# Kernel optimization log

Measured on AMD Instinct MI355X. Metric: run time of the kernel, lower is better.

Reference implementation:

```python
import jax, jax.numpy as jnp
import numpy as np

# ---- MPDM social-force hyperparameters (the `param` object in the torch code) ----
N = 4096            # number of agents (agent 0 = robot)
PED_SPEED = 1.5     # param.pedestrians_speed (max / desired speed, m/s)
ROBOT_SPEED = 1.5   # param.robot_speed
K = 2.0             # param.k   (goal-attraction relaxation gain)
ALPHA = 10.0        # param.alpha (repulsive force amplitude)
PED_RADIUS = 0.3    # param.ped_radius
PED_MASS = 60.0     # param.ped_mass
BETTA = 0.71        # param.betta (repulsive range)
DT = 0.4            # param.DT
A_COST = 4.0        # param.a (progress weight)
B_COST = 1.2        # param.b (blame range)
E_COST = 0.001      # param.e (numerical epsilon)
EPS = 1e-8


def setup_inputs() -> dict:
    key = jax.random.key(0)
    k1, k2, k3, k4 = jax.random.split(key, 4)
    pos = jax.random.normal(k1, (N, 2), dtype=jnp.float32) * 10.0   # spread agents over ~20x20 m
    vel = jax.random.normal(k2, (N, 2), dtype=jnp.float32) * 0.5
    state = jnp.concatenate([pos, vel], axis=1)                     # [N,4] = (x, y, vx, vy)
    goals = jax.random.normal(k3, (N, 2), dtype=jnp.float32) * 10.0
    cost = jnp.zeros((N, 1), dtype=jnp.float32)
    stacked = state                                                 # trajectory stack seed
    robot_init_pose = jax.random.normal(k4, (2,), dtype=jnp.float32) * 10.0
    return {"state": state, "cost": cost,
            "stacked_trajectories_for_visualizer": stacked,
            "goals": goals, "robot_init_pose": robot_init_pose}


def calc_forces(state, goals):
    pos = state[:, 0:2]
    vel = state[:, 2:4]
    # --- attractive force: relax toward desired velocity pointing at goal ---
    to_goal = goals - pos                                   # [N,2]
    dist_goal = jnp.linalg.norm(to_goal, axis=1, keepdims=True)
    e_goal = to_goal / (dist_goal + EPS)
    desired_speed = jnp.full((N, 1), PED_SPEED, dtype=state.dtype).at[0, 0].set(ROBOT_SPEED)
    attr_force = K * (desired_speed * e_goal - vel) * PED_MASS      # [N,2]
    # --- repulsive force: all-pairs exponential social force ---
    diff = pos[:, None, :] - pos[None, :, :]                # [N,N,2]
    d = jnp.sqrt(jnp.sum(diff * diff, axis=-1) + EPS)       # [N,N]
    n_ij = diff / d[..., None]                              # unit vectors
    mag = ALPHA * jnp.exp((2.0 * PED_RADIUS - d) / BETTA)   # [N,N]
    mag = mag * (1.0 - jnp.eye(N, dtype=state.dtype))       # no self-force
    rep_force = jnp.sum(mag[..., None] * n_ij, axis=1)      # [N,2]
    return rep_force, attr_force


def pose_propagation(F, state):
    pos = state[:, 0:2]
    vel = state[:, 2:4]
    vel_new = vel + (F / PED_MASS) * DT
    speed = jnp.linalg.norm(vel_new, axis=1, keepdims=True)
    # clamp speed to max pedestrian speed
    vel_new = vel_new * jnp.minimum(1.0, PED_SPEED / (speed + EPS))
    pos_new = pos + vel_new * DT
    return jnp.concatenate([pos_new, vel_new], axis=1)      # [N,4]


def calc_cost_function(goals, robot_init_pose, state_out):
    pos = state_out[:, 0:2]
    robot_pose = pos[0]
    # robot progress toward its goal (projection onto initial goal direction)
    goal_dir = goals[0] - robot_init_pose
    PG = jnp.dot(goal_dir, robot_pose - robot_init_pose) / (jnp.linalg.norm(goal_dir) + E_COST)
    # blame: pedestrians close to the robot
    dist_to_robot = jnp.sqrt(jnp.sum((pos - robot_pose) ** 2, axis=1) + E_COST)
    blame = jnp.exp(-dist_to_robot / B_COST)
    blame = blame.at[0].set(0.0)                            # robot does not blame itself
    return -A_COST * PG + blame                             # [N]


def reference(state, cost, stacked_trajectories_for_visualizer, goals, robot_init_pose):
    rf, af = calc_forces(state, goals)
    F = rf + af
    out = pose_propagation(F, state)
    temp = calc_cost_function(goals, robot_init_pose, out)
    new_cost = cost + temp.reshape(-1, 1)
    stacked = jnp.concatenate([stacked_trajectories_for_visualizer, state], axis=0)
    return (out, new_cost, stacked)
```

## Files before the change

### kernel.cpp

```cpp
#include <hip/hip_runtime.h>

#define NN 4096
#define CHUNK 64
#define NCHUNK (NN / CHUNK)

__global__ __launch_bounds__(256) void rep_partial(const float* __restrict__ state,
                                                   float2* __restrict__ part) {
    __shared__ float2 sp[CHUNK];
    const int i = blockIdx.x * 256 + threadIdx.x;
    const int jbase = blockIdx.y * CHUNK;
    if (threadIdx.x < CHUNK) {
        float4 s = reinterpret_cast<const float4*>(state)[jbase + threadIdx.x];
        sp[threadIdx.x] = make_float2(s.x, s.y);
    }
    __syncthreads();

    const float4 me = reinterpret_cast<const float4*>(state)[i];
    const float px = me.x, py = me.y;
    float fx = 0.f, fy = 0.f;

    const float C1E = 2.0319648462f;
    const float C0E = 4.5411071f;

#pragma unroll 16
    for (int t = 0; t < CHUNK; ++t) {
        float2 q = sp[t];
        float dx = px - q.x;
        float dy = py - q.y;
        float d2 = fmaf(dx, dx, 1e-8f);
        d2 = fmaf(dy, dy, d2);
        float inv_d = __builtin_amdgcn_rsqf(d2);
        float d = d2 * inv_d;
        float e = __builtin_amdgcn_exp2f(fmaf(-C1E, d, C0E));
        float w = e * inv_d;
        fx = fmaf(w, dx, fx);
        fy = fmaf(w, dy, fy);
    }
    part[blockIdx.y * NN + i] = make_float2(fx, fy);
}

__global__ __launch_bounds__(256) void propagate(const float* __restrict__ state,
                                                 const float* __restrict__ goals,
                                                 const float2* __restrict__ part,
                                                 float* __restrict__ out_state,
                                                 float* __restrict__ stacked_second) {
    const int i = blockIdx.x * 256 + threadIdx.x;

    float Fx = 0.f, Fy = 0.f;
#pragma unroll
    for (int c = 0; c < NCHUNK; ++c) {
        float2 p = part[c * NN + i];
        Fx += p.x;
        Fy += p.y;
    }

    const float4 me = reinterpret_cast<const float4*>(state)[i];
    const float2 g  = reinterpret_cast<const float2*>(goals)[i];

    float tgx = g.x - me.x, tgy = g.y - me.y;
    float dist = sqrtf(tgx * tgx + tgy * tgy);
    float inv = 1.f / (dist + 1e-8f);
    Fx += 180.f * (tgx * inv) - 120.f * me.z;
    Fy += 180.f * (tgy * inv) - 120.f * me.w;

    float vnx = me.z + Fx * (0.4f / 60.f);
    float vny = me.w + Fy * (0.4f / 60.f);
    float speed = sqrtf(vnx * vnx + vny * vny);
    float scale = fminf(1.f, 1.5f / (speed + 1e-8f));
    vnx *= scale;
    vny *= scale;
    float pnx = me.x + vnx * 0.4f;
    float pny = me.y + vny * 0.4f;

    reinterpret_cast<float4*>(out_state)[i]      = make_float4(pnx, pny, vnx, vny);
    reinterpret_cast<float4*>(stacked_second)[i] = me;
}

__global__ __launch_bounds__(256) void cost_and_copy(const float* __restrict__ out_state,
                                                     const float* __restrict__ cost_in,
                                                     const float* __restrict__ goals,
                                                     const float* __restrict__ robot_init,
                                                     const float* __restrict__ stacked_in,
                                                     float* __restrict__ cost_out,
                                                     float* __restrict__ stacked_first) {
    const int i = blockIdx.x * 256 + threadIdx.x;

    float rx = out_state[0], ry = out_state[1];
    float r0x = robot_init[0], r0y = robot_init[1];
    float gdx = goals[0] - r0x, gdy = goals[1] - r0y;
    float PG = (gdx * (rx - r0x) + gdy * (ry - r0y))
             / (sqrtf(gdx * gdx + gdy * gdy) + 0.001f);

    float px = out_state[4 * i], py = out_state[4 * i + 1];
    float ddx = px - rx, ddy = py - ry;
    float dist = sqrtf(ddx * ddx + ddy * ddy + 0.001f);
    float blame = (i == 0) ? 0.f
                : __builtin_amdgcn_exp2f(dist * -1.2022458675f);

    cost_out[i] = cost_in[i] + (-4.f * PG + blame);
    reinterpret_cast<float4*>(stacked_first)[i] =
        reinterpret_cast<const float4*>(stacked_in)[i];
}

extern "C" void kernel_launch(void* const* d_in, const int* in_sizes, int n_in,
                              void* d_out, int out_size, void* d_ws, size_t ws_size,
                              hipStream_t stream) {
    const float* state      = (const float*)d_in[0];
    const float* cost       = (const float*)d_in[1];
    const float* stacked_in = (const float*)d_in[2];
    const float* goals      = (const float*)d_in[3];
    const float* robot_init = (const float*)d_in[4];

    float* out          = (float*)d_out;
    float* out_state    = out;
    float* out_cost     = out + NN * 4;
    float* out_stacked  = out + NN * 5;

    float2* part = (float2*)d_ws;

    dim3 gridA(NN / 256, NCHUNK);
    rep_partial<<<gridA, 256, 0, stream>>>(state, part);

    propagate<<<NN / 256, 256, 0, stream>>>(state, goals, part,
                                            out_state, out_stacked + NN * 4);

    cost_and_copy<<<NN / 256, 256, 0, stream>>>(out_state, cost, goals, robot_init,
                                                stacked_in, out_cost, out_stacked);
}
```

Measured before the change: 72.38 us.

## Fuse force, propagation and cost into one kernel with wave-per-agent reduction

Replaces the three-kernel pipeline and its partial-force workspace with a single kernel. Each 1024-thread block loads all positions into shared memory and assigns one wave per agent, reducing pair forces with cross-lane shuffles. Every block redundantly recomputes the robot's force and new pose so the cost term no longer needs a separate launch. This removes two launches and the partial-sum round trip through global memory, at the cost of extra per-block robot work and a full 32 KB shared-memory fill in each of 256 blocks.

```diff
diff --git a/kernel.cpp b/kernel.cpp
--- a/kernel.cpp
+++ b/kernel.cpp
@@ -1,105 +1,123 @@
 #include <hip/hip_runtime.h>
 
 #define NN 4096
-#define CHUNK 64
-#define NCHUNK (NN / CHUNK)
 
-__global__ __launch_bounds__(256) void rep_partial(const float* __restrict__ state,
-                                                   float2* __restrict__ part) {
-    __shared__ float2 sp[CHUNK];
-    const int i = blockIdx.x * 256 + threadIdx.x;
-    const int jbase = blockIdx.y * CHUNK;
-    if (threadIdx.x < CHUNK) {
-        float4 s = reinterpret_cast<const float4*>(state)[jbase + threadIdx.x];
-        sp[threadIdx.x] = make_float2(s.x, s.y);
+__device__ inline float4 propagate_one(float2 pos, float2 vel, float2 goal, float2 F) {
+    float tgx = goal.x - pos.x, tgy = goal.y - pos.y;
+    float dist = sqrtf(tgx * tgx + tgy * tgy);
+    float inv = 1.f / (dist + 1e-8f);
+    float Fx = F.x + 180.f * (tgx * inv) - 120.f * vel.x;
+    float Fy = F.y + 180.f * (tgy * inv) - 120.f * vel.y;
+    float vnx = vel.x + Fx * (0.4f / 60.f);
+    float vny = vel.y + Fy * (0.4f / 60.f);
+    float sp = sqrtf(vnx * vnx + vny * vny);
+    float sc = fminf(1.f, 1.5f / (sp + 1e-8f));
+    vnx *= sc; vny *= sc;
+    return make_float4(pos.x + vnx * 0.4f, pos.y + vny * 0.4f, vnx, vny);
+}
+
+__global__ __launch_bounds__(1024) void fused_step(
+    const float* __restrict__ state, const float* __restrict__ cost_in,
+    const float* __restrict__ stacked_in, const float* __restrict__ goals,
+    const float* __restrict__ robot_init,
+    float* __restrict__ out_state, float* __restrict__ out_cost,
+    float* __restrict__ out_stacked)
+{
+    __shared__ float2 sp[NN];
+    __shared__ float2 sF[16];
+    __shared__ float2 sR[16];
+    __shared__ float2 sPN[16];
+    __shared__ float2 sRobot;
+
+    const int tid = threadIdx.x;
+
+#pragma unroll
+    for (int k = 0; k < 4; ++k) {
+        int idx = tid + k * 1024;
+        float4 s = reinterpret_cast<const float4*>(state)[idx];
+        sp[idx] = make_float2(s.x, s.y);
     }
     __syncthreads();
 
-    const float4 me = reinterpret_cast<const float4*>(state)[i];
-    const float px = me.x, py = me.y;
-    float fx = 0.f, fy = 0.f;
+    const int wave = tid >> 6, lane = tid & 63;
+    const int i = blockIdx.x * 16 + wave;
+    const float2 pi = sp[i];
+    const float2 p0 = sp[0];
 
     const float C1E = 2.0319648462f;
     const float C0E = 4.5411071f;
 
-#pragma unroll 16
-    for (int t = 0; t < CHUNK; ++t) {
-        float2 q = sp[t];
-        float dx = px - q.x;
-        float dy = py - q.y;
-        float d2 = fmaf(dx, dx, 1e-8f);
-        d2 = fmaf(dy, dy, d2);
+    float fx = 0.f, fy = 0.f, rfx = 0.f, rfy = 0.f;
+#pragma unroll 8
+    for (int t = 0; t < 64; ++t) {
+        float2 q = sp[t * 64 + lane];
+        float dx = pi.x - q.x, dy = pi.y - q.y;
+        float d2 = fmaf(dy, dy, fmaf(dx, dx, 1e-8f));
         float inv_d = __builtin_amdgcn_rsqf(d2);
-        float d = d2 * inv_d;
-        float e = __builtin_amdgcn_exp2f(fmaf(-C1E, d, C0E));
+        float e = __builtin_amdgcn_exp2f(fmaf(-C1E, d2 * inv_d, C0E));
         float w = e * inv_d;
-        fx = fmaf(w, dx, fx);
-        fy = fmaf(w, dy, fy);
+        fx = fmaf(w, dx, fx); fy = fmaf(w, dy, fy);
     }
-    part[blockIdx.y * NN + i] = make_float2(fx, fy);
-}
+#pragma unroll
+    for (int t = 0; t < 4; ++t) {
+        float2 q = sp[wave * 256 + t * 64 + lane];
+        float dx = p0.x - q.x, dy = p0.y - q.y;
+        float d2 = fmaf(dy, dy, fmaf(dx, dx, 1e-8f));
+        float inv_d = __builtin_amdgcn_rsqf(d2);
+        float e = __builtin_amdgcn_exp2f(fmaf(-C1E, d2 * inv_d, C0E));
+        float w = e * inv_d;
+        rfx = fmaf(w, dx, rfx); rfy = fmaf(w, dy, rfy);
+    }
+#pragma unroll
+    for (int off = 32; off > 0; off >>= 1) {
+        fx  += __shfl_xor(fx,  off);
+        fy  += __shfl_xor(fy,  off);
+        rfx += __shfl_xor(rfx, off);
+        rfy += __shfl_xor(rfy, off);
+    }
+    if (lane == 0) { sF[wave] = make_float2(fx, fy); sR[wave] = make_float2(rfx, rfy); }
+    __syncthreads();
 
-__global__ __launch_bounds__(256) void propagate(const float* __restrict__ state,
-                                                 const float* __restrict__ goals,
-                                                 const float2* __restrict__ part,
-                                                 float* __restrict__ out_state,
-                                                 float* __restrict__ stacked_second) {
-    const int i = blockIdx.x * 256 + threadIdx.x;
+    if (tid < 16) {
+        int iw = blockIdx.x * 16 + tid;
+        float4 s = reinterpret_cast<const float4*>(state)[iw];
+        float2 g = reinterpret_cast<const float2*>(goals)[iw];
+        float4 r = propagate_one(make_float2(s.x, s.y), make_float2(s.z, s.w), g, sF[tid]);
+        reinterpret_cast<float4*>(out_state)[iw] = r;
+        sPN[tid] = make_float2(r.x, r.y);
+    } else if (tid == 31) {
+        float2 F0 = make_float2(0.f, 0.f);
+#pragma unroll
+        for (int c = 0; c < 16; ++c) { F0.x += sR[c].x; F0.y += sR[c].y; }
+        float4 s0 = reinterpret_cast<const float4*>(state)[0];
+        float2 g0 = reinterpret_cast<const float2*>(goals)[0];
+        float4 r = propagate_one(make_float2(s0.x, s0.y), make_float2(s0.z, s0.w), g0, F0);
+        sRobot = make_float2(r.x, r.y);
+    } else if (tid >= 64 && tid < 80) {
+        int iw = blockIdx.x * 16 + (tid - 64);
+        reinterpret_cast<float4*>(out_stacked)[NN + iw] =
+            reinterpret_cast<const float4*>(state)[iw];
+    } else if (tid >= 128 && tid < 144) {
+        int iw = blockIdx.x * 16 + (tid - 128);
+        reinterpret_cast<float4*>(out_stacked)[iw] =
+            reinterpret_cast<const float4*>(stacked_in)[iw];
+    }
+    __syncthreads();
 
-    float Fx = 0.f, Fy = 0.f;
-#pragma unroll
-    for (int c = 0; c < NCHUNK; ++c) {
-        float2 p = part[c * NN + i];
-        Fx += p.x;
-        Fy += p.y;
+    if (tid < 16) {
+        int iw = blockIdx.x * 16 + tid;
+        float2 rp = sRobot;
+        float r0x = robot_init[0], r0y = robot_init[1];
+        float gdx = goals[0] - r0x, gdy = goals[1] - r0y;
+        float PG = (gdx * (rp.x - r0x) + gdy * (rp.y - r0y))
+                 / (sqrtf(gdx * gdx + gdy * gdy) + 0.001f);
+        float2 pn = sPN[tid];
+        float ddx = pn.x - rp.x, ddy = pn.y - rp.y;
+        float dist = sqrtf(ddx * ddx + ddy * ddy + 0.001f);
+        float blame = (iw == 0) ? 0.f
+                    : __builtin_amdgcn_exp2f(dist * -1.2022458675f);
+        out_cost[iw] = cost_in[iw] + (-4.f * PG + blame);
     }
-
-    const float4 me = reinterpret_cast<const float4*>(state)[i];
-    const float2 g  = reinterpret_cast<const float2*>(goals)[i];
-
-    float tgx = g.x - me.x, tgy = g.y - me.y;
-    float dist = sqrtf(tgx * tgx + tgy * tgy);
-    float inv = 1.f / (dist + 1e-8f);
-    Fx += 180.f * (tgx * inv) - 120.f * me.z;
-    Fy += 180.f * (tgy * inv) - 120.f * me.w;
-
-    float vnx = me.z + Fx * (0.4f / 60.f);
-    float vny = me.w + Fy * (0.4f / 60.f);
-    float speed = sqrtf(vnx * vnx + vny * vny);
-    float scale = fminf(1.f, 1.5f / (speed + 1e-8f));
-    vnx *= scale;
-    vny *= scale;
-    float pnx = me.x + vnx * 0.4f;
-    float pny = me.y + vny * 0.4f;
-
-    reinterpret_cast<float4*>(out_state)[i]      = make_float4(pnx, pny, vnx, vny);
-    reinterpret_cast<float4*>(stacked_second)[i] = me;
-}
-
-__global__ __launch_bounds__(256) void cost_and_copy(const float* __restrict__ out_state,
-                                                     const float* __restrict__ cost_in,
-                                                     const float* __restrict__ goals,
-                                                     const float* __restrict__ robot_init,
-                                                     const float* __restrict__ stacked_in,
-                                                     float* __restrict__ cost_out,
-                                                     float* __restrict__ stacked_first) {
-    const int i = blockIdx.x * 256 + threadIdx.x;
-
-    float rx = out_state[0], ry = out_state[1];
-    float r0x = robot_init[0], r0y = robot_init[1];
-    float gdx = goals[0] - r0x, gdy = goals[1] - r0y;
-    float PG = (gdx * (rx - r0x) + gdy * (ry - r0y))
-             / (sqrtf(gdx * gdx + gdy * gdy) + 0.001f);
-
-    float px = out_state[4 * i], py = out_state[4 * i + 1];
-    float ddx = px - rx, ddy = py - ry;
-    float dist = sqrtf(ddx * ddx + ddy * ddy + 0.001f);
-    float blame = (i == 0) ? 0.f
-                : __builtin_amdgcn_exp2f(dist * -1.2022458675f);
-
-    cost_out[i] = cost_in[i] + (-4.f * PG + blame);
-    reinterpret_cast<float4*>(stacked_first)[i] =
-        reinterpret_cast<const float4*>(stacked_in)[i];
 }
 
 extern "C" void kernel_launch(void* const* d_in, const int* in_sizes, int n_in,
@@ -111,19 +129,12 @@
     const float* goals      = (const float*)d_in[3];
     const float* robot_init = (const float*)d_in[4];
 
-    float* out          = (float*)d_out;
-    float* out_state    = out;
-    float* out_cost     = out + NN * 4;
-    float* out_stacked  = out + NN * 5;
+    float* out         = (float*)d_out;
+    float* out_state   = out;
+    float* out_cost    = out + NN * 4;
+    float* out_stacked = out + NN * 5;
 
-    float2* part = (float2*)d_ws;
-
-    dim3 gridA(NN / 256, NCHUNK);
-    rep_partial<<<gridA, 256, 0, stream>>>(state, part);
-
-    propagate<<<NN / 256, 256, 0, stream>>>(state, goals, part,
-                                            out_state, out_stacked + NN * 4);
-
-    cost_and_copy<<<NN / 256, 256, 0, stream>>>(out_state, cost, goals, robot_init,
-                                                stacked_in, out_cost, out_stacked);
+    fused_step<<<NN / 16, 1024, 0, stream>>>(state, cost, stacked_in, goals,
+                                             robot_init, out_state, out_cost,
+                                             out_stacked);
 }
```

New measurement: 69.09 us. -4.6%, faster.
